# Kernel tuning notes

Hardware: AMD Instinct MI355X
Metric: run time of the kernel (lower is better)

Reference implementation:

```python
import jax, jax.numpy as jnp
import numpy as np

B, T, C = 2, 4096, 768
H = 12
HD = C // H  # 64


def setup_inputs() -> dict:
    key = jax.random.key(0)
    k1, k2, k3 = jax.random.split(key, 3)
    scale = 0.02
    x = jax.random.normal(k1, (B, T, C), dtype=jnp.float32)
    w_attn = jax.random.normal(k2, (C, 3 * C), dtype=jnp.float32) * scale
    b_attn = jnp.zeros((3 * C,), dtype=jnp.float32)
    w_proj = jax.random.normal(k3, (C, C), dtype=jnp.float32) * scale
    b_proj = jnp.zeros((C,), dtype=jnp.float32)
    return {"x": x, "w_attn": w_attn, "b_attn": b_attn,
            "w_proj": w_proj, "b_proj": b_proj}


def reference(x, w_attn, b_attn, w_proj, b_proj):
    b, t, c = x.shape
    # QKV projection: (B,T,3C)
    qkv = x @ w_attn + b_attn
    q, k, v = jnp.split(qkv, 3, axis=2)
    # (B,H,T,HD)
    q = q.reshape(b, t, H, HD).transpose(0, 2, 1, 3)
    k = k.reshape(b, t, H, HD).transpose(0, 2, 1, 3)
    v = v.reshape(b, t, H, HD).transpose(0, 2, 1, 3)
    # scores: (B,H,T,T)
    scores = jnp.einsum('bhqd,bhkd->bhqk', q, k) / jnp.sqrt(jnp.float32(HD))
    causal = jnp.tril(jnp.ones((t, t), dtype=bool))
    scores = jnp.where(causal[None, None, :, :], scores, -jnp.inf)
    att = jax.nn.softmax(scores, axis=-1)
    # attn_dropout p=0 -> identity
    y = jnp.einsum('bhqk,bhkd->bhqd', att, v)
    y = y.transpose(0, 2, 1, 3).reshape(b, t, c)
    # output projection (resid_dropout p=0 -> identity)
    return y @ w_proj + b_proj
```

## Files before the change

### kernel.cpp

```cpp
#include <hip/hip_runtime.h>


typedef unsigned short u16;
typedef unsigned int u32;
using bf16x8 = __attribute__((ext_vector_type(8))) short;
using f32x4  = __attribute__((ext_vector_type(4))) float;

__device__ __forceinline__ float bf2f(u16 u) {
  return __uint_as_float(((u32)u) << 16);
}
__device__ __forceinline__ u16 f2bf(float f) {
  u32 u = __float_as_uint(f);
  u += 0x7fffu + ((u >> 16) & 1u);
  return (u16)(u >> 16);
}
__device__ __forceinline__ u32 cvtpk(float lo, float hi) {
  u32 r;
  asm("v_cvt_pk_bf16_f32 %0, %1, %2" : "=v"(r) : "v"(lo), "v"(hi));
  return r;
}
__device__ __forceinline__ void gload_lds16(const u16* g, u16* l) {
  __builtin_amdgcn_global_load_lds(
      (const __attribute__((address_space(1))) unsigned int*)g,
      (__attribute__((address_space(3))) unsigned int*)l, 16, 0, 0);
}

__global__ void fill_sentinel_f32(float* __restrict__ out, int n, float v) {
  const int i0 = blockIdx.x * blockDim.x + threadIdx.x;
  const int stride = gridDim.x * blockDim.x;
  for (int i = i0; i < n; i += stride) out[i] = v;
}

__global__ void convert_f32_bf16(const float* __restrict__ src, u16* __restrict__ dst,
                                 int n) {
  const int i0 = blockIdx.x * blockDim.x + threadIdx.x;
  const int stride = gridDim.x * blockDim.x;
  for (int i = i0; i < n; i += stride) dst[i] = f2bf(src[i]);
}

__global__ void transpose_f32_bf16(const float* __restrict__ in, u16* __restrict__ out,
                                   int R, int C) {
  __shared__ u16 tile[32][33];
  const int c0 = blockIdx.x * 32, r0 = blockIdx.y * 32;
  const int tx = threadIdx.x & 31, ty = threadIdx.x >> 5;
#pragma unroll
  for (int i = 0; i < 32; i += 8)
    tile[ty + i][tx] = f2bf(in[(size_t)(r0 + ty + i) * C + c0 + tx]);
  __syncthreads();
#pragma unroll
  for (int i = 0; i < 32; i += 8)
    out[(size_t)(c0 + ty + i) * R + r0 + tx] = tile[tx][ty + i];
}

#define LDT 72
#define QSCALE 0.18033688011112f

__device__ __forceinline__ void stage_tile(u16* lds, const u16* g, int ld, int tid) {
#pragma unroll
  for (int i = 0; i < 4; ++i) {
    const int idx = i * 256 + tid;
    const int r = idx >> 3, c = (idx & 7) * 8;
    *(uint4*)&lds[r * LDT + c] = *(const uint4*)&g[(size_t)r * ld + c];
  }
}

template <int MODE>
__global__ __launch_bounds__(256, 2)
void gemm128(const u16* __restrict__ A, const u16* __restrict__ Bt,
             const u16* __restrict__ bias, void* __restrict__ O0v,
             u16* __restrict__ O1, u16* __restrict__ O2, int Kd) {
  __shared__ __align__(16) u16 As[128 * LDT];
  __shared__ __align__(16) u16 Bs[128 * LDT];
  const int tid = threadIdx.x;
  const int lane = tid & 63, wave = tid >> 6;
  const int wm = wave >> 1, wn = wave & 1;
  const int l16 = lane & 15, quad = lane >> 4;

  const u16* Ag = A + (size_t)blockIdx.x * 128 * Kd;
  const u16* Bg = Bt + (size_t)blockIdx.y * 128 * Kd;

  f32x4 acc[4][4] = {};
  for (int kt = 0; kt < Kd; kt += 64) {
    stage_tile(As, Ag + kt, Kd, tid);
    stage_tile(Bs, Bg + kt, Kd, tid);
    __syncthreads();
#pragma unroll
    for (int s = 0; s < 2; ++s) {
      bf16x8 af[4], bfr[4];
#pragma unroll
      for (int i = 0; i < 4; ++i) {
        const int m = wm * 64 + i * 16 + l16;
        af[i] = *(const bf16x8*)&As[m * LDT + (s * 4 + quad) * 8];
        const int n = wn * 64 + i * 16 + l16;
        bfr[i] = *(const bf16x8*)&Bs[n * LDT + (s * 4 + quad) * 8];
      }
#pragma unroll
      for (int i = 0; i < 4; ++i)
#pragma unroll
        for (int j = 0; j < 4; ++j)
          acc[i][j] = __builtin_amdgcn_mfma_f32_16x16x32_bf16(af[i], bfr[j],
                                                              acc[i][j], 0, 0, 0);
    }
    __syncthreads();
  }

#pragma unroll
  for (int i = 0; i < 4; ++i) {
    const int mbase = blockIdx.x * 128 + wm * 64 + i * 16 + quad * 4;
#pragma unroll
    for (int j = 0; j < 4; ++j) {
      const int nb = blockIdx.y * 128 + wn * 64 + j * 16;
      const int n = nb + l16;
      const float bv = bf2f(bias[n]);
      if (MODE == 0) {
        const int which = nb / 768;
        const int b = mbase >> 12, t = mbase & 4095;
        const int c = n - which * 768;
        const int h = c >> 6, d = c & 63;
        const size_t bh = (size_t)b * 12 + h;
        if (which == 0) {
#pragma unroll
          for (int r = 0; r < 4; ++r)
            ((u16*)O0v)[((bh * 4096 + t + r) << 6) + d] =
                f2bf((acc[i][j][r] + bv) * QSCALE);
        } else if (which == 1) {
#pragma unroll
          for (int r = 0; r < 4; ++r)
            O1[((bh * 4096 + t + r) << 6) + d] = f2bf(acc[i][j][r] + bv);
        } else {
          ushort4 pk;
          pk.x = f2bf(acc[i][j][0] + bv);
          pk.y = f2bf(acc[i][j][1] + bv);
          pk.z = f2bf(acc[i][j][2] + bv);
          pk.w = f2bf(acc[i][j][3] + bv);
          *(ushort4*)&O2[((bh << 6) + (size_t)d) * 4096 + t] = pk;
        }
      } else {
#pragma unroll
        for (int r = 0; r < 4; ++r)
          ((float*)O0v)[(size_t)(mbase + r) * 768 + n] = acc[i][j][r] + bv;
      }
    }
  }
}

__global__ __launch_bounds__(256, 4)
void attn_chunk(const u16* __restrict__ Q, const u16* __restrict__ K,
                const u16* __restrict__ Vt, u16* __restrict__ Y,
                u16* __restrict__ part_o, float* __restrict__ part_l) {
  const int idx = blockIdx.x;
  const int bh = idx % 24;
  const int cid = 79 - (idx / 24);
  int qt = 0, base = 0, nc = 1;
  for (int q = 0; q < 32; ++q) {
    const int c = (q >> 3) + 1;
    if (cid < base + c) { qt = q; nc = c; break; }
    base += c;
  }
  const int j = cid - base;
  const int Nt = 2 * qt + 2;
  const int kbeg = j * 16;
  const int kend = (kbeg + 16 < Nt) ? kbeg + 16 : Nt;
  const int q0 = qt * 128;
  const int b = bh / 12, h = bh % 12;
  const size_t ho = (size_t)bh * 4096 * 64;
  const u16* Qg = Q + ho + (size_t)q0 * 64;
  const u16* Kg = K + ho;
  const u16* Vg = Vt + ho;

  __shared__ __align__(16) u16 Ks[2][64 * 64];
  __shared__ __align__(16) u16 Vs[2][64 * 64];

  const int tid = threadIdx.x;
  const int lane = tid & 63, wave = tid >> 6;
  const int l16 = lane & 15, quad = lane >> 4;
  const int sw8 = (l16 & 7) * 8;

  const int rl = tid >> 3, m7 = tid & 7;
  const int cs = (m7 ^ (rl & 7)) * 8;
  const u16* kg0 = Kg + (size_t)rl * 64 + cs;
  const u16* vg0 = Vg + (size_t)rl * 4096 + cs;
  const int wb = wave * 512;

  bf16x8 qf[2][2];
#pragma unroll
  for (int rt = 0; rt < 2; ++rt)
#pragma unroll
    for (int s = 0; s < 2; ++s)
      qf[rt][s] = *(const bf16x8*)&Qg[(wave * 32 + rt * 16 + l16) * 64 + s * 32 + quad * 8];

  bf16x8 ones;
#pragma unroll
  for (int e = 0; e < 8; ++e) ones[e] = (short)0x3F80;

  f32x4 lacc[2] = {};
  f32x4 o[2][4] = {};

  auto stage = [&](int bf, int kt2) {
    const size_t ko = (size_t)kt2 * 4096;
    const int to = kt2 * 64;
    gload_lds16(kg0 + ko,               &Ks[bf][wb]);
    gload_lds16(kg0 + ko + 2048,        &Ks[bf][2048 + wb]);
    gload_lds16(vg0 + to,               &Vs[bf][wb]);
    gload_lds16(vg0 + to + 32 * 4096,   &Vs[bf][2048 + wb]);
  };

  stage(0, kbeg);
  __syncthreads();
  int cur = 0;

  for (int kt2 = kbeg; kt2 < kend; ++kt2) {
    const int t0 = kt2 * 64;
    const bool more = (kt2 + 1 < kend);
    if (more) stage(cur ^ 1, kt2 + 1);

    f32x4 sc[4][2] = {};
#pragma unroll
    for (int s = 0; s < 2; ++s) {
      bf16x8 kf[4];
#pragma unroll
      for (int nt = 0; nt < 4; ++nt)
        kf[nt] = *(const bf16x8*)&Ks[cur][(nt * 16 + l16) * 64 +
                                          ((s * 32 + quad * 8) ^ sw8)];
#pragma unroll
      for (int nt = 0; nt < 4; ++nt)
#pragma unroll
        for (int rt = 0; rt < 2; ++rt)
          sc[nt][rt] = __builtin_amdgcn_mfma_f32_16x16x32_bf16(kf[nt], qf[rt][s],
                                                               sc[nt][rt], 0, 0, 0);
    }

    u32 pw[4][2][2];
#pragma unroll
    for (int rt = 0; rt < 2; ++rt) {
      const int rowb = q0 + wave * 32 + rt * 16;
      if (t0 + 63 <= rowb) {
#pragma unroll
        for (int nt = 0; nt < 4; ++nt) {
          f32x4 p;
#pragma unroll
          for (int r = 0; r < 4; ++r)
            p[r] = __builtin_amdgcn_exp2f(sc[nt][rt][r]);
          pw[nt][rt][0] = cvtpk(p[0], p[1]);
          pw[nt][rt][1] = cvtpk(p[2], p[3]);
        }
      } else {
        const int qrow = rowb + l16;
#pragma unroll
        for (int nt = 0; nt < 4; ++nt) {
          f32x4 p;
#pragma unroll
          for (int r = 0; r < 4; ++r) {
            float pv = __builtin_amdgcn_exp2f(sc[nt][rt][r]);
            if (t0 + nt * 16 + quad * 4 + r > qrow) pv = 0.f;
            p[r] = pv;
          }
          pw[nt][rt][0] = cvtpk(p[0], p[1]);
          pw[nt][rt][1] = cvtpk(p[2], p[3]);
        }
      }
    }

#pragma unroll
    for (int s2 = 0; s2 < 2; ++s2) {
      bf16x8 vf[4];
#pragma unroll
      for (int dt = 0; dt < 4; ++dt) {
        const int vbase = (dt * 16 + l16) * 64;
        const int a1 = vbase + ((s2 * 32 + quad * 4) ^ sw8);
        union { uint2 hv[2]; bf16x8 v; } uv;
        uv.hv[0] = *(const uint2*)&Vs[cur][a1];
        uv.hv[1] = *(const uint2*)&Vs[cur][a1 ^ 16];
        vf[dt] = uv.v;
      }
#pragma unroll
      for (int rt = 0; rt < 2; ++rt) {
        union { u32 w[4]; bf16x8 v; } up;
        up.w[0] = pw[2 * s2][rt][0];
        up.w[1] = pw[2 * s2][rt][1];
        up.w[2] = pw[2 * s2 + 1][rt][0];
        up.w[3] = pw[2 * s2 + 1][rt][1];
#pragma unroll
        for (int dt = 0; dt < 4; ++dt)
          o[rt][dt] = __builtin_amdgcn_mfma_f32_16x16x32_bf16(up.v, vf[dt],
                                                              o[rt][dt], 0, 0, 0);
        lacc[rt] = __builtin_amdgcn_mfma_f32_16x16x32_bf16(up.v, ones,
                                                           lacc[rt], 0, 0, 0);
      }
    }

    if (more) {
      __syncthreads();
      cur ^= 1;
    }
  }

  if (nc == 1) {
#pragma unroll
    for (int rt = 0; rt < 2; ++rt)
#pragma unroll
      for (int r = 0; r < 4; ++r) {
        const float inv = 1.f / lacc[rt][r];
        const int t = q0 + wave * 32 + rt * 16 + quad * 4 + r;
#pragma unroll
        for (int dt = 0; dt < 4; ++dt)
          Y[((size_t)b * 4096 + t) * 768 + h * 64 + dt * 16 + l16] =
              f2bf(o[rt][dt][r] * inv);
      }
  } else {
    const int pslot = bh * 72 + (cid - 8);
    u16* po = part_o + (size_t)pslot * 8192;
    float* pl = part_l + pslot * 128;
#pragma unroll
    for (int rt = 0; rt < 2; ++rt)
#pragma unroll
      for (int r = 0; r < 4; ++r) {
        const int row = wave * 32 + rt * 16 + quad * 4 + r;
#pragma unroll
        for (int dt = 0; dt < 4; ++dt)
          po[row * 64 + dt * 16 + l16] = f2bf(o[rt][dt][r]);
        if (l16 == 0) pl[row] = lacc[rt][r];
      }
  }
}

__global__ __launch_bounds__(256, 8)
void attn_combine(const u16* __restrict__ part_o, const float* __restrict__ part_l,
                  u16* __restrict__ Y) {
  const int bh = blockIdx.x, qt = 8 + blockIdx.y;
  const int g = qt >> 3, i = qt & 7;
  const int nc = g + 1;
  const int base = 4 * g * (g + 1) + i * (g + 1);
  const int slot0 = bh * 72 + base - 8;
  const int b = bh / 12, h = bh % 12;
  const int q0 = qt * 128;
  for (int e = threadIdx.x; e < 8192; e += 256) {
    const int row = e >> 6, d = e & 63;
    float Os = 0.f, ls = 0.f;
    for (int c = 0; c < nc; ++c) {
      Os += bf2f(part_o[(size_t)(slot0 + c) * 8192 + e]);
      ls += part_l[(slot0 + c) * 128 + row];
    }
    Y[((size_t)b * 4096 + q0 + row) * 768 + h * 64 + d] = f2bf(Os / ls);
  }
}

extern "C" void kernel_launch(void* const* d_in, const int* in_sizes, int n_in,
                              void* d_out, int out_size, void* d_ws, size_t ws_size,
                              hipStream_t stream) {
  (void)in_sizes; (void)n_in;
  const float* x      = (const float*)d_in[0];
  const float* w_attn = (const float*)d_in[1];
  const float* b_attn = (const float*)d_in[2];
  const float* w_proj = (const float*)d_in[3];
  const float* b_proj = (const float*)d_in[4];
  float* out = (float*)d_out;

  char* ws = (char*)d_ws;
  size_t off = 0;
  auto alloc = [&](size_t bytes) -> void* {
    void* p = ws + off;
    off += (bytes + 255) & ~(size_t)255;
    return p;
  };
  u16* xb  = (u16*)alloc((size_t)8192 * 768 * 2);
  u16* WtA = (u16*)alloc((size_t)2304 * 768 * 2);
  u16* WtP = (u16*)alloc((size_t)768 * 768 * 2);
  u16* ba  = (u16*)alloc(2304 * 2);
  u16* bp  = (u16*)alloc(768 * 2);
  u16* Q   = (u16*)alloc((size_t)6291456 * 2);
  u16* Kp  = (u16*)alloc((size_t)6291456 * 2);
  u16* Vt  = (u16*)alloc((size_t)6291456 * 2);
  u16* Y   = (u16*)alloc((size_t)6291456 * 2);
  u16* part_o  = (u16*)alloc((size_t)24 * 72 * 8192 * 2);
  float* part_l = (float*)alloc((size_t)24 * 72 * 128 * 4);

  if (ws_size < off) {
    fill_sentinel_f32<<<256, 256, 0, stream>>>(out, out_size,
                                               100.0f + (float)(ws_size >> 20));
    return;
  }

  convert_f32_bf16<<<2048, 256, 0, stream>>>(x, xb, 8192 * 768);
  convert_f32_bf16<<<16, 256, 0, stream>>>(b_attn, ba, 2304);
  convert_f32_bf16<<<8, 256, 0, stream>>>(b_proj, bp, 768);
  transpose_f32_bf16<<<dim3(72, 24), 256, 0, stream>>>(w_attn, WtA, 768, 2304);
  transpose_f32_bf16<<<dim3(24, 24), 256, 0, stream>>>(w_proj, WtP, 768, 768);

  gemm128<0><<<dim3(64, 18), 256, 0, stream>>>(xb, WtA, ba, Q, Kp, Vt, 768);
  attn_chunk<<<1920, 256, 0, stream>>>(Q, Kp, Vt, Y, part_o, part_l);
  attn_combine<<<dim3(24, 24), 256, 0, stream>>>(part_o, part_l, Y);
  gemm128<1><<<dim3(64, 6), 256, 0, stream>>>(Y, WtP, bp, out, nullptr, nullptr, 768);
}
```

Baseline: 277.0 us.

## Triple-buffer K/V LDS tiles with vmcnt-based waits and MFMA priority boosts

Changes the attention chunk kernel from double to triple buffering of K/V tiles in LDS, prefetching two tiles ahead. Each step now waits with explicit s_waitcnt vmcnt counters and a raw s_barrier instead of __syncthreads, so the most recent prefetch can stay in flight. MFMA sections are wrapped in s_setprio raises so the matrix cores get issue priority. The extra LDS (48KB per block) lowers the occupancy target from 4 to 3 blocks per CU, which may cut latency hiding across blocks.

```diff
diff --git a/kernel.cpp b/kernel.cpp
--- a/kernel.cpp
+++ b/kernel.cpp
@@ -144,7 +144,7 @@
   }
 }
 
-__global__ __launch_bounds__(256, 4)
+__global__ __launch_bounds__(256, 3)
 void attn_chunk(const u16* __restrict__ Q, const u16* __restrict__ K,
                 const u16* __restrict__ Vt, u16* __restrict__ Y,
                 u16* __restrict__ part_o, float* __restrict__ part_l) {
@@ -168,8 +168,8 @@
   const u16* Kg = K + ho;
   const u16* Vg = Vt + ho;
 
-  __shared__ __align__(16) u16 Ks[2][64 * 64];
-  __shared__ __align__(16) u16 Vs[2][64 * 64];
+  __shared__ __align__(16) u16 Ks[3][64 * 64];
+  __shared__ __align__(16) u16 Vs[3][64 * 64];
 
   const int tid = threadIdx.x;
   const int lane = tid & 63, wave = tid >> 6;
@@ -205,14 +205,26 @@
     gload_lds16(vg0 + to + 32 * 4096,   &Vs[bf][2048 + wb]);
   };
 
+  const int ntt = kend - kbeg;
   stage(0, kbeg);
-  __syncthreads();
+  if (ntt > 1) {
+    stage(1, kbeg + 1);
+    asm volatile("s_waitcnt vmcnt(4)" ::: "memory");
+  } else {
+    asm volatile("s_waitcnt vmcnt(0)" ::: "memory");
+  }
+  __builtin_amdgcn_sched_barrier(0);
+  __builtin_amdgcn_s_barrier();
   int cur = 0;
 
   for (int kt2 = kbeg; kt2 < kend; ++kt2) {
     const int t0 = kt2 * 64;
-    const bool more = (kt2 + 1 < kend);
-    if (more) stage(cur ^ 1, kt2 + 1);
+    const bool pf = (kt2 + 2 < kend);
+    if (pf) {
+      int nb = cur + 2; if (nb >= 3) nb -= 3;
+      stage(nb, kt2 + 2);
+    }
+    __builtin_amdgcn_sched_barrier(0);
 
     f32x4 sc[4][2] = {};
 #pragma unroll
@@ -222,12 +234,14 @@
       for (int nt = 0; nt < 4; ++nt)
         kf[nt] = *(const bf16x8*)&Ks[cur][(nt * 16 + l16) * 64 +
                                           ((s * 32 + quad * 8) ^ sw8)];
+      __builtin_amdgcn_s_setprio(1);
 #pragma unroll
       for (int nt = 0; nt < 4; ++nt)
 #pragma unroll
         for (int rt = 0; rt < 2; ++rt)
           sc[nt][rt] = __builtin_amdgcn_mfma_f32_16x16x32_bf16(kf[nt], qf[rt][s],
                                                                sc[nt][rt], 0, 0, 0);
+      __builtin_amdgcn_s_setprio(0);
     }
 
     u32 pw[4][2][2];
@@ -280,18 +294,23 @@
         up.w[1] = pw[2 * s2][rt][1];
         up.w[2] = pw[2 * s2 + 1][rt][0];
         up.w[3] = pw[2 * s2 + 1][rt][1];
+        __builtin_amdgcn_s_setprio(1);
 #pragma unroll
         for (int dt = 0; dt < 4; ++dt)
           o[rt][dt] = __builtin_amdgcn_mfma_f32_16x16x32_bf16(up.v, vf[dt],
                                                               o[rt][dt], 0, 0, 0);
         lacc[rt] = __builtin_amdgcn_mfma_f32_16x16x32_bf16(up.v, ones,
                                                            lacc[rt], 0, 0, 0);
-      }
-    }
-
-    if (more) {
-      __syncthreads();
-      cur ^= 1;
+        __builtin_amdgcn_s_setprio(0);
+      }
+    }
+
+    if (kt2 + 1 < kend) {
+      if (pf) asm volatile("s_waitcnt vmcnt(4)" ::: "memory");
+      else    asm volatile("s_waitcnt vmcnt(0)" ::: "memory");
+      __builtin_amdgcn_sched_barrier(0);
+      __builtin_amdgcn_s_barrier();
+      if (++cur == 3) cur = 0;
     }
   }
 
```

Measured after the change: 271.1 us. -2.1%, faster.
